# Performance work log

Measured on AMD Instinct MI355X. Metric: run time of the kernel, lower is better.

## Reference

```python
import jax, jax.numpy as jnp
import numpy as np

N_NODES = 50000
N_EDGES = 640000
HIDDEN = 128
NUM_CONVS = 3
VOCAB = 100  # nn.Embedding(100, hidden_dim)


def setup_inputs() -> dict:
    key = jax.random.key(0)
    ks = jax.random.split(key, 8)
    z = jax.random.randint(ks[0], (N_NODES,), 0, VOCAB)
    edge_index = jax.random.randint(ks[1], (2, N_EDGES), 0, N_NODES)
    edge_attr = jax.random.normal(ks[2], (N_EDGES, HIDDEN), jnp.float32)
    emb = jax.random.normal(ks[3], (VOCAB, HIDDEN), jnp.float32) * 0.02
    s = 1.0 / np.sqrt(HIDDEN)
    # Stacked per-conv MLP params: Linear(H,H) -> relu -> Linear(H,H)
    W1 = jax.random.uniform(ks[4], (NUM_CONVS, HIDDEN, HIDDEN), jnp.float32, -s, s)
    b1 = jnp.zeros((NUM_CONVS, HIDDEN), jnp.float32)
    W2 = jax.random.uniform(ks[5], (NUM_CONVS, HIDDEN, HIDDEN), jnp.float32, -s, s)
    b2 = jnp.zeros((NUM_CONVS, HIDDEN), jnp.float32)
    return dict(z=z, edge_index=edge_index, edge_attr=edge_attr,
                emb=emb, W1=W1, b1=b1, W2=W2, b2=b2)


def reference(z, edge_index, edge_attr, emb, W1, b1, W2, b2):
    x = emb[z]  # [N, H] node embeddings
    src, dst = edge_index[0], edge_index[1]
    n = x.shape[0]
    num_convs = W1.shape[0]
    for i in range(num_convs):
        # GINEConv: message = relu(x_j + edge_attr), aggr='add' at dst
        msg = jax.nn.relu(x[src] + edge_attr)                      # [E, H]
        agg = jax.ops.segment_sum(msg, dst, num_segments=n)        # [N, H]
        out = agg + x  # (1 + eps) * x_r with eps = 0
        # MultiLayerPerceptron(H, [H, H], activation='relu'): relu between layers only
        h = jax.nn.relu(out @ W1[i] + b1[i]) @ W2[i] + b2[i]
        if i < num_convs - 1:
            h = jax.nn.relu(h)  # inter-conv activation
        x = h + x  # short_cut residual
    return x  # concat_hidden=False -> last hidden
```

## Files before the change

### kernel.cpp

```cpp
#include <hip/hip_runtime.h>

#define HID 128
#define NNODE 50000
#define NEDGE 640000

static __global__ void embed_kernel(const int* __restrict__ z,
                                    const float* __restrict__ emb,
                                    float* __restrict__ x) {
  int i = blockIdx.x * 256 + threadIdx.x;
  const int total = NNODE * (HID / 4);
  if (i >= total) return;
  int node = i >> 5;
  int c = i & 31;
  ((float4*)x)[i] = ((const float4*)emb)[(size_t)z[node] * 32 + c];
}

static __global__ void hist_kernel(const int* __restrict__ dst, int* __restrict__ deg) {
  int i = blockIdx.x * 256 + threadIdx.x;
  if (i < NEDGE) atomicAdd(&deg[dst[i]], 1);
}

static __global__ void scan_kernel(const int* __restrict__ deg,
                                   int* __restrict__ row_ptr,
                                   int* __restrict__ cursor) {
  __shared__ int sums[1024];
  int t = threadIdx.x;
  const int per = (NNODE + 1023) / 1024;
  int base = t * per;
  int s = 0;
  for (int i = 0; i < per; ++i) {
    int idx = base + i;
    if (idx < NNODE) s += deg[idx];
  }
  sums[t] = s;
  __syncthreads();
  for (int off = 1; off < 1024; off <<= 1) {
    int v = (t >= off) ? sums[t - off] : 0;
    __syncthreads();
    if (t >= off) sums[t] += v;
    __syncthreads();
  }
  int run = (t == 0) ? 0 : sums[t - 1];
  for (int i = 0; i < per; ++i) {
    int idx = base + i;
    if (idx < NNODE) {
      row_ptr[idx] = run;
      cursor[idx] = run;
      run += deg[idx];
    }
  }
  if (t == 1023) row_ptr[NNODE] = run;
}

static __global__ void fill_kernel(const int* __restrict__ src, const int* __restrict__ dst,
                                   int* __restrict__ cursor, int2* __restrict__ elist) {
  int i = blockIdx.x * 256 + threadIdx.x;
  if (i < NEDGE) {
    int d = dst[i];
    int p = atomicAdd(&cursor[d], 1);
    elist[p] = make_int2(i, src[i]);
  }
}

static __global__ __launch_bounds__(256) void gather_kernel(
    const float* __restrict__ x, const float* __restrict__ ea,
    const int* __restrict__ row_ptr, const int2* __restrict__ elist,
    float* __restrict__ out) {
  int wave = threadIdx.x >> 6;
  int lane = threadIdx.x & 63;
  int node = blockIdx.x * 4 + wave;
  if (node >= NNODE) return;
  const float2* x2 = (const float2*)x;
  const float2* e2 = (const float2*)ea;
  float2 a0 = x2[(size_t)node * 64 + lane];
  float2 a1 = make_float2(0.f, 0.f);
  float2 a2 = make_float2(0.f, 0.f);
  float2 a3 = make_float2(0.f, 0.f);
  int j  = row_ptr[node];
  int je = row_ptr[node + 1];
  for (; j + 4 <= je; j += 4) {
    int2 e0 = elist[j], e1 = elist[j + 1], e2i = elist[j + 2], e3 = elist[j + 3];
    float2 xv0 = x2[(size_t)e0.y * 64 + lane];
    float2 ev0 = e2[(size_t)e0.x * 64 + lane];
    float2 xv1 = x2[(size_t)e1.y * 64 + lane];
    float2 ev1 = e2[(size_t)e1.x * 64 + lane];
    float2 xv2 = x2[(size_t)e2i.y * 64 + lane];
    float2 ev2 = e2[(size_t)e2i.x * 64 + lane];
    float2 xv3 = x2[(size_t)e3.y * 64 + lane];
    float2 ev3 = e2[(size_t)e3.x * 64 + lane];
    a0.x += fmaxf(xv0.x + ev0.x, 0.f); a0.y += fmaxf(xv0.y + ev0.y, 0.f);
    a1.x += fmaxf(xv1.x + ev1.x, 0.f); a1.y += fmaxf(xv1.y + ev1.y, 0.f);
    a2.x += fmaxf(xv2.x + ev2.x, 0.f); a2.y += fmaxf(xv2.y + ev2.y, 0.f);
    a3.x += fmaxf(xv3.x + ev3.x, 0.f); a3.y += fmaxf(xv3.y + ev3.y, 0.f);
  }
  for (; j < je; ++j) {
    int2 es = elist[j];
    float2 xv = x2[(size_t)es.y * 64 + lane];
    float2 ev = e2[(size_t)es.x * 64 + lane];
    a0.x += fmaxf(xv.x + ev.x, 0.f);
    a0.y += fmaxf(xv.y + ev.y, 0.f);
  }
  a0.x += a1.x + a2.x + a3.x;
  a0.y += a1.y + a2.y + a3.y;
  ((float2*)out)[(size_t)node * 64 + lane] = a0;
}

static __global__ __launch_bounds__(256) void mlp_kernel(
    const float* __restrict__ in, const float* __restrict__ xres,
    const float* __restrict__ W1, const float* __restrict__ b1,
    const float* __restrict__ W2, const float* __restrict__ b2,
    float* __restrict__ xout, int relu_out) {
  __shared__ float As[64 * 132];
  __shared__ float Wb[32 * 128];
  const int tid = threadIdx.x;
  const int row0 = blockIdx.x * 64;

  for (int i = tid; i < 64 * 32; i += 256) {
    int r = i >> 5, c = i & 31;
    float4 v = make_float4(0.f, 0.f, 0.f, 0.f);
    int row = row0 + r;
    if (row < NNODE) v = ((const float4*)in)[(size_t)row * 32 + c];
    *(float4*)&As[r * 132 + c * 4] = v;
  }

  const int rg = tid >> 4, cg = tid & 15;
  const int rb = rg * 4, cb = cg * 8;

  float acc[4][8];
#pragma unroll
  for (int r = 0; r < 4; ++r)
#pragma unroll
    for (int c = 0; c < 8; ++c) acc[r][c] = 0.f;

  for (int ch = 0; ch < 4; ++ch) {
    __syncthreads();
    for (int i = tid; i < 32 * 32; i += 256)
      ((float4*)Wb)[i] = ((const float4*)(W1 + ch * 32 * 128))[i];
    __syncthreads();
    const int k0 = ch * 32;
    for (int k = 0; k < 32; k += 4) {
      float4 a0 = *(const float4*)&As[(rb + 0) * 132 + k0 + k];
      float4 a1 = *(const float4*)&As[(rb + 1) * 132 + k0 + k];
      float4 a2 = *(const float4*)&As[(rb + 2) * 132 + k0 + k];
      float4 a3 = *(const float4*)&As[(rb + 3) * 132 + k0 + k];
#pragma unroll
      for (int kk = 0; kk < 4; ++kk) {
        float4 w0 = *(const float4*)&Wb[(k + kk) * 128 + cb];
        float4 w1 = *(const float4*)&Wb[(k + kk) * 128 + cb + 4];
        float av[4] = {((const float*)&a0)[kk], ((const float*)&a1)[kk],
                       ((const float*)&a2)[kk], ((const float*)&a3)[kk]};
#pragma unroll
        for (int r = 0; r < 4; ++r) {
          acc[r][0] += av[r] * w0.x; acc[r][1] += av[r] * w0.y;
          acc[r][2] += av[r] * w0.z; acc[r][3] += av[r] * w0.w;
          acc[r][4] += av[r] * w1.x; acc[r][5] += av[r] * w1.y;
          acc[r][6] += av[r] * w1.z; acc[r][7] += av[r] * w1.w;
        }
      }
    }
  }
  __syncthreads();

  {
    float4 bb0 = ((const float4*)b1)[cb >> 2];
    float4 bb1 = ((const float4*)b1)[(cb >> 2) + 1];
    float bv[8] = {bb0.x, bb0.y, bb0.z, bb0.w, bb1.x, bb1.y, bb1.z, bb1.w};
#pragma unroll
    for (int r = 0; r < 4; ++r) {
      float t0[8];
#pragma unroll
      for (int c = 0; c < 8; ++c) t0[c] = fmaxf(acc[r][c] + bv[c], 0.f);
      *(float4*)&As[(rb + r) * 132 + cb]     = make_float4(t0[0], t0[1], t0[2], t0[3]);
      *(float4*)&As[(rb + r) * 132 + cb + 4] = make_float4(t0[4], t0[5], t0[6], t0[7]);
    }
  }

#pragma unroll
  for (int r = 0; r < 4; ++r)
#pragma unroll
    for (int c = 0; c < 8; ++c) acc[r][c] = 0.f;

  for (int ch = 0; ch < 4; ++ch) {
    __syncthreads();
    for (int i = tid; i < 32 * 32; i += 256)
      ((float4*)Wb)[i] = ((const float4*)(W2 + ch * 32 * 128))[i];
    __syncthreads();
    const int k0 = ch * 32;
    for (int k = 0; k < 32; k += 4) {
      float4 a0 = *(const float4*)&As[(rb + 0) * 132 + k0 + k];
      float4 a1 = *(const float4*)&As[(rb + 1) * 132 + k0 + k];
      float4 a2 = *(const float4*)&As[(rb + 2) * 132 + k0 + k];
      float4 a3 = *(const float4*)&As[(rb + 3) * 132 + k0 + k];
#pragma unroll
      for (int kk = 0; kk < 4; ++kk) {
        float4 w0 = *(const float4*)&Wb[(k + kk) * 128 + cb];
        float4 w1 = *(const float4*)&Wb[(k + kk) * 128 + cb + 4];
        float av[4] = {((const float*)&a0)[kk], ((const float*)&a1)[kk],
                       ((const float*)&a2)[kk], ((const float*)&a3)[kk]};
#pragma unroll
        for (int r = 0; r < 4; ++r) {
          acc[r][0] += av[r] * w0.x; acc[r][1] += av[r] * w0.y;
          acc[r][2] += av[r] * w0.z; acc[r][3] += av[r] * w0.w;
          acc[r][4] += av[r] * w1.x; acc[r][5] += av[r] * w1.y;
          acc[r][6] += av[r] * w1.z; acc[r][7] += av[r] * w1.w;
        }
      }
    }
  }

  {
    float4 bb0 = ((const float4*)b2)[cb >> 2];
    float4 bb1 = ((const float4*)b2)[(cb >> 2) + 1];
    float bv[8] = {bb0.x, bb0.y, bb0.z, bb0.w, bb1.x, bb1.y, bb1.z, bb1.w};
#pragma unroll
    for (int r = 0; r < 4; ++r) {
      int row = row0 + rb + r;
      if (row < NNODE) {
        float4 xv0 = ((const float4*)xres)[(size_t)row * 32 + (cb >> 2)];
        float4 xv1 = ((const float4*)xres)[(size_t)row * 32 + (cb >> 2) + 1];
        float o[8];
#pragma unroll
        for (int c = 0; c < 8; ++c) {
          float v = acc[r][c] + bv[c];
          if (relu_out) v = fmaxf(v, 0.f);
          o[c] = v;
        }
        o[0] += xv0.x; o[1] += xv0.y; o[2] += xv0.z; o[3] += xv0.w;
        o[4] += xv1.x; o[5] += xv1.y; o[6] += xv1.z; o[7] += xv1.w;
        ((float4*)xout)[(size_t)row * 32 + (cb >> 2)]     = make_float4(o[0], o[1], o[2], o[3]);
        ((float4*)xout)[(size_t)row * 32 + (cb >> 2) + 1] = make_float4(o[4], o[5], o[6], o[7]);
      }
    }
  }
}

extern "C" void kernel_launch(void* const* d_in, const int* in_sizes, int n_in,
                              void* d_out, int out_size, void* d_ws, size_t ws_size,
                              hipStream_t stream) {
  const int*   z   = (const int*)d_in[0];
  const int*   ei  = (const int*)d_in[1];
  const float* ea  = (const float*)d_in[2];
  const float* emb = (const float*)d_in[3];
  const float* W1  = (const float*)d_in[4];
  const float* b1  = (const float*)d_in[5];
  const float* W2  = (const float*)d_in[6];
  const float* b2  = (const float*)d_in[7];
  float* outp = (float*)d_out;

  char* ws = (char*)d_ws;
  float* xbuf   = (float*)(ws + 0);
  float* obuf   = (float*)(ws + 25600000);
  int*   deg    = (int*)  (ws + 51200000);
  int*   cursor = (int*)  (ws + 51400000);
  int*   rowptr = (int*)  (ws + 51600000);
  int2*  elist  = (int2*) (ws + 51800016);

  const int* srcv = ei;
  const int* dstv = ei + NEDGE;

  hipMemsetAsync(deg, 0, NNODE * sizeof(int), stream);
  embed_kernel<<<(NNODE * 32 + 255) / 256, 256, 0, stream>>>(z, emb, xbuf);
  hist_kernel<<<(NEDGE + 255) / 256, 256, 0, stream>>>(dstv, deg);
  scan_kernel<<<1, 1024, 0, stream>>>(deg, rowptr, cursor);
  fill_kernel<<<(NEDGE + 255) / 256, 256, 0, stream>>>(srcv, dstv, cursor, elist);

  for (int i = 0; i < 3; ++i) {
    gather_kernel<<<(NNODE + 3) / 4, 256, 0, stream>>>(xbuf, ea, rowptr, elist, obuf);
    float* xo = (i == 2) ? outp : xbuf;
    mlp_kernel<<<(NNODE + 63) / 64, 256, 0, stream>>>(
        obuf, xbuf,
        W1 + (size_t)i * HID * HID, b1 + (size_t)i * HID,
        W2 + (size_t)i * HID * HID, b2 + (size_t)i * HID,
        xo, (i < 2) ? 1 : 0);
  }
}
```

Before: 1.076 ms.

## Run node MLP on bf16 MFMA with split-precision weights and activations

Result: faster. 967.5 us (-10.1%).

```diff
diff --git a/kernel.cpp b/kernel.cpp
--- a/kernel.cpp
+++ b/kernel.cpp
@@ -3,6 +3,9 @@
 #define HID 128
 #define NNODE 50000
 #define NEDGE 640000
+
+typedef __attribute__((ext_vector_type(8))) short bf16x8;
+typedef __attribute__((ext_vector_type(4))) float f32x4;
 
 static __global__ void embed_kernel(const int* __restrict__ z,
                                     const float* __restrict__ emb,
@@ -62,6 +65,25 @@
   }
 }
 
+static __global__ void wsplit_kernel(const float* __restrict__ W1, const float* __restrict__ W2,
+                                     unsigned short* __restrict__ whi,
+                                     unsigned short* __restrict__ wlo) {
+  int idx = blockIdx.x * 256 + threadIdx.x;
+  if (idx >= 6 * 16384) return;
+  int cg = idx >> 14;
+  int rem = idx & 16383;
+  int k = rem >> 7, n = rem & 127;
+  int c = cg >> 1, g = cg & 1;
+  float v = (g ? W2 : W1)[c * 16384 + k * 128 + n];
+  unsigned u = __float_as_uint(v);
+  unsigned hb = u >> 16;
+  float hf = __uint_as_float(hb << 16);
+  unsigned lb = __float_as_uint(v - hf) >> 16;
+  int o = cg * 17408 + n * 136 + k;
+  whi[o] = (unsigned short)hb;
+  wlo[o] = (unsigned short)lb;
+}
+
 static __global__ __launch_bounds__(256) void gather_kernel(
     const float* __restrict__ x, const float* __restrict__ ea,
     const int* __restrict__ row_ptr, const int2* __restrict__ elist,
@@ -71,7 +93,7 @@
   int node = blockIdx.x * 4 + wave;
   if (node >= NNODE) return;
   const float2* x2 = (const float2*)x;
-  const float2* e2 = (const float2*)ea;
+  const double* ed = (const double*)ea;
   float2 a0 = x2[(size_t)node * 64 + lane];
   float2 a1 = make_float2(0.f, 0.f);
   float2 a2 = make_float2(0.f, 0.f);
@@ -81,13 +103,15 @@
   for (; j + 4 <= je; j += 4) {
     int2 e0 = elist[j], e1 = elist[j + 1], e2i = elist[j + 2], e3 = elist[j + 3];
     float2 xv0 = x2[(size_t)e0.y * 64 + lane];
-    float2 ev0 = e2[(size_t)e0.x * 64 + lane];
+    double d0 = __builtin_nontemporal_load(&ed[(size_t)e0.x * 64 + lane]);
     float2 xv1 = x2[(size_t)e1.y * 64 + lane];
-    float2 ev1 = e2[(size_t)e1.x * 64 + lane];
+    double d1 = __builtin_nontemporal_load(&ed[(size_t)e1.x * 64 + lane]);
     float2 xv2 = x2[(size_t)e2i.y * 64 + lane];
-    float2 ev2 = e2[(size_t)e2i.x * 64 + lane];
+    double d2 = __builtin_nontemporal_load(&ed[(size_t)e2i.x * 64 + lane]);
     float2 xv3 = x2[(size_t)e3.y * 64 + lane];
-    float2 ev3 = e2[(size_t)e3.x * 64 + lane];
+    double d3 = __builtin_nontemporal_load(&ed[(size_t)e3.x * 64 + lane]);
+    float2 ev0 = *(float2*)&d0, ev1 = *(float2*)&d1;
+    float2 ev2 = *(float2*)&d2, ev3 = *(float2*)&d3;
     a0.x += fmaxf(xv0.x + ev0.x, 0.f); a0.y += fmaxf(xv0.y + ev0.y, 0.f);
     a1.x += fmaxf(xv1.x + ev1.x, 0.f); a1.y += fmaxf(xv1.y + ev1.y, 0.f);
     a2.x += fmaxf(xv2.x + ev2.x, 0.f); a2.y += fmaxf(xv2.y + ev2.y, 0.f);
@@ -96,7 +120,8 @@
   for (; j < je; ++j) {
     int2 es = elist[j];
     float2 xv = x2[(size_t)es.y * 64 + lane];
-    float2 ev = e2[(size_t)es.x * 64 + lane];
+    double d0 = __builtin_nontemporal_load(&ed[(size_t)es.x * 64 + lane]);
+    float2 ev = *(float2*)&d0;
     a0.x += fmaxf(xv.x + ev.x, 0.f);
     a0.y += fmaxf(xv.y + ev.y, 0.f);
   }
@@ -105,130 +130,123 @@
   ((float2*)out)[(size_t)node * 64 + lane] = a0;
 }
 
-static __global__ __launch_bounds__(256) void mlp_kernel(
+static __global__ __launch_bounds__(256) void mlp_mfma(
     const float* __restrict__ in, const float* __restrict__ xres,
-    const float* __restrict__ W1, const float* __restrict__ b1,
-    const float* __restrict__ W2, const float* __restrict__ b2,
+    const unsigned short* __restrict__ wt1hi, const unsigned short* __restrict__ wt1lo,
+    const unsigned short* __restrict__ wt2hi, const unsigned short* __restrict__ wt2lo,
+    const float* __restrict__ b1, const float* __restrict__ b2,
     float* __restrict__ xout, int relu_out) {
-  __shared__ float As[64 * 132];
-  __shared__ float Wb[32 * 128];
+  __shared__ unsigned short WbHi[128 * 72];
+  __shared__ unsigned short WbLo[128 * 72];
+  __shared__ float Ts[64 * 132];
   const int tid = threadIdx.x;
+  const int w = tid >> 6, l = tid & 63;
+  const int lm = l & 15, quad = l >> 4;
   const int row0 = blockIdx.x * 64;
 
-  for (int i = tid; i < 64 * 32; i += 256) {
-    int r = i >> 5, c = i & 31;
-    float4 v = make_float4(0.f, 0.f, 0.f, 0.f);
-    int row = row0 + r;
-    if (row < NNODE) v = ((const float4*)in)[(size_t)row * 32 + c];
-    *(float4*)&As[r * 132 + c * 4] = v;
-  }
-
-  const int rg = tid >> 4, cg = tid & 15;
-  const int rb = rg * 4, cb = cg * 8;
-
-  float acc[4][8];
-#pragma unroll
-  for (int r = 0; r < 4; ++r)
-#pragma unroll
-    for (int c = 0; c < 8; ++c) acc[r][c] = 0.f;
-
-  for (int ch = 0; ch < 4; ++ch) {
-    __syncthreads();
-    for (int i = tid; i < 32 * 32; i += 256)
-      ((float4*)Wb)[i] = ((const float4*)(W1 + ch * 32 * 128))[i];
-    __syncthreads();
-    const int k0 = ch * 32;
-    for (int k = 0; k < 32; k += 4) {
-      float4 a0 = *(const float4*)&As[(rb + 0) * 132 + k0 + k];
-      float4 a1 = *(const float4*)&As[(rb + 1) * 132 + k0 + k];
-      float4 a2 = *(const float4*)&As[(rb + 2) * 132 + k0 + k];
-      float4 a3 = *(const float4*)&As[(rb + 3) * 132 + k0 + k];
-#pragma unroll
-      for (int kk = 0; kk < 4; ++kk) {
-        float4 w0 = *(const float4*)&Wb[(k + kk) * 128 + cb];
-        float4 w1 = *(const float4*)&Wb[(k + kk) * 128 + cb + 4];
-        float av[4] = {((const float*)&a0)[kk], ((const float*)&a1)[kk],
-                       ((const float*)&a2)[kk], ((const float*)&a3)[kk]};
-#pragma unroll
-        for (int r = 0; r < 4; ++r) {
-          acc[r][0] += av[r] * w0.x; acc[r][1] += av[r] * w0.y;
-          acc[r][2] += av[r] * w0.z; acc[r][3] += av[r] * w0.w;
-          acc[r][4] += av[r] * w1.x; acc[r][5] += av[r] * w1.y;
-          acc[r][6] += av[r] * w1.z; acc[r][7] += av[r] * w1.w;
-        }
+  float b1v[8], b2v[8];
+#pragma unroll
+  for (int t = 0; t < 8; ++t) { b1v[t] = b1[t * 16 + lm]; b2v[t] = b2[t * 16 + lm]; }
+
+  f32x4 acc[8];
+#pragma unroll
+  for (int t = 0; t < 8; ++t) acc[t] = (f32x4){0.f, 0.f, 0.f, 0.f};
+
+  int arow = row0 + w * 16 + lm;
+  if (arow >= NNODE) arow = NNODE - 1;
+
+  for (int kc = 0; kc < 128; kc += 64) {
+    __syncthreads();
+    for (int idx = tid; idx < 128 * 8; idx += 256) {
+      int n = idx >> 3, seg = idx & 7;
+      *(uint4*)&WbHi[n * 72 + seg * 8] = *(const uint4*)&wt1hi[n * 136 + kc + seg * 8];
+      *(uint4*)&WbLo[n * 72 + seg * 8] = *(const uint4*)&wt1lo[n * 136 + kc + seg * 8];
+    }
+    __syncthreads();
+#pragma unroll
+    for (int ks = 0; ks < 64; ks += 32) {
+      const float* ap = in + (size_t)arow * 128 + kc + ks + quad * 8;
+      float4 av0 = *(const float4*)ap;
+      float4 av1 = *(const float4*)(ap + 4);
+      float av[8] = {av0.x, av0.y, av0.z, av0.w, av1.x, av1.y, av1.z, av1.w};
+      bf16x8 ah, al;
+#pragma unroll
+      for (int jj = 0; jj < 8; ++jj) {
+        unsigned u = __float_as_uint(av[jj]);
+        unsigned hb = u >> 16;
+        float hf = __uint_as_float(hb << 16);
+        unsigned lb = __float_as_uint(av[jj] - hf) >> 16;
+        ah[jj] = (short)hb; al[jj] = (short)lb;
+      }
+#pragma unroll
+      for (int t = 0; t < 8; ++t) {
+        int off = (t * 16 + lm) * 72 + ks + quad * 8;
+        bf16x8 bh = *(const bf16x8*)&WbHi[off];
+        bf16x8 bl = *(const bf16x8*)&WbLo[off];
+        acc[t] = __builtin_amdgcn_mfma_f32_16x16x32_bf16(ah, bh, acc[t], 0, 0, 0);
+        acc[t] = __builtin_amdgcn_mfma_f32_16x16x32_bf16(ah, bl, acc[t], 0, 0, 0);
+        acc[t] = __builtin_amdgcn_mfma_f32_16x16x32_bf16(al, bh, acc[t], 0, 0, 0);
       }
     }
   }
   __syncthreads();
 
-  {
-    float4 bb0 = ((const float4*)b1)[cb >> 2];
-    float4 bb1 = ((const float4*)b1)[(cb >> 2) + 1];
-    float bv[8] = {bb0.x, bb0.y, bb0.z, bb0.w, bb1.x, bb1.y, bb1.z, bb1.w};
+#pragma unroll
+  for (int t = 0; t < 8; ++t)
+#pragma unroll
+    for (int r = 0; r < 4; ++r)
+      Ts[(w * 16 + quad * 4 + r) * 132 + t * 16 + lm] = fmaxf(acc[t][r] + b1v[t], 0.f);
+
+#pragma unroll
+  for (int t = 0; t < 8; ++t) acc[t] = (f32x4){0.f, 0.f, 0.f, 0.f};
+  __syncthreads();
+
+  for (int kc = 0; kc < 128; kc += 64) {
+    __syncthreads();
+    for (int idx = tid; idx < 128 * 8; idx += 256) {
+      int n = idx >> 3, seg = idx & 7;
+      *(uint4*)&WbHi[n * 72 + seg * 8] = *(const uint4*)&wt2hi[n * 136 + kc + seg * 8];
+      *(uint4*)&WbLo[n * 72 + seg * 8] = *(const uint4*)&wt2lo[n * 136 + kc + seg * 8];
+    }
+    __syncthreads();
+#pragma unroll
+    for (int ks = 0; ks < 64; ks += 32) {
+      const float* tp = &Ts[(w * 16 + lm) * 132 + kc + ks + quad * 8];
+      float4 av0 = *(const float4*)tp;
+      float4 av1 = *(const float4*)(tp + 4);
+      float av[8] = {av0.x, av0.y, av0.z, av0.w, av1.x, av1.y, av1.z, av1.w};
+      bf16x8 ah, al;
+#pragma unroll
+      for (int jj = 0; jj < 8; ++jj) {
+        unsigned u = __float_as_uint(av[jj]);
+        unsigned hb = u >> 16;
+        float hf = __uint_as_float(hb << 16);
+        unsigned lb = __float_as_uint(av[jj] - hf) >> 16;
+        ah[jj] = (short)hb; al[jj] = (short)lb;
+      }
+#pragma unroll
+      for (int t = 0; t < 8; ++t) {
+        int off = (t * 16 + lm) * 72 + ks + quad * 8;
+        bf16x8 bh = *(const bf16x8*)&WbHi[off];
+        bf16x8 bl = *(const bf16x8*)&WbLo[off];
+        acc[t] = __builtin_amdgcn_mfma_f32_16x16x32_bf16(ah, bh, acc[t], 0, 0, 0);
+        acc[t] = __builtin_amdgcn_mfma_f32_16x16x32_bf16(ah, bl, acc[t], 0, 0, 0);
+        acc[t] = __builtin_amdgcn_mfma_f32_16x16x32_bf16(al, bh, acc[t], 0, 0, 0);
+      }
+    }
+  }
+
+#pragma unroll
+  for (int t = 0; t < 8; ++t) {
 #pragma unroll
     for (int r = 0; r < 4; ++r) {
-      float t0[8];
-#pragma unroll
-      for (int c = 0; c < 8; ++c) t0[c] = fmaxf(acc[r][c] + bv[c], 0.f);
-      *(float4*)&As[(rb + r) * 132 + cb]     = make_float4(t0[0], t0[1], t0[2], t0[3]);
-      *(float4*)&As[(rb + r) * 132 + cb + 4] = make_float4(t0[4], t0[5], t0[6], t0[7]);
-    }
-  }
-
-#pragma unroll
-  for (int r = 0; r < 4; ++r)
-#pragma unroll
-    for (int c = 0; c < 8; ++c) acc[r][c] = 0.f;
-
-  for (int ch = 0; ch < 4; ++ch) {
-    __syncthreads();
-    for (int i = tid; i < 32 * 32; i += 256)
-      ((float4*)Wb)[i] = ((const float4*)(W2 + ch * 32 * 128))[i];
-    __syncthreads();
-    const int k0 = ch * 32;
-    for (int k = 0; k < 32; k += 4) {
-      float4 a0 = *(const float4*)&As[(rb + 0) * 132 + k0 + k];
-      float4 a1 = *(const float4*)&As[(rb + 1) * 132 + k0 + k];
-      float4 a2 = *(const float4*)&As[(rb + 2) * 132 + k0 + k];
-      float4 a3 = *(const float4*)&As[(rb + 3) * 132 + k0 + k];
-#pragma unroll
-      for (int kk = 0; kk < 4; ++kk) {
-        float4 w0 = *(const float4*)&Wb[(k + kk) * 128 + cb];
-        float4 w1 = *(const float4*)&Wb[(k + kk) * 128 + cb + 4];
-        float av[4] = {((const float*)&a0)[kk], ((const float*)&a1)[kk],
-                       ((const float*)&a2)[kk], ((const float*)&a3)[kk]};
-#pragma unroll
-        for (int r = 0; r < 4; ++r) {
-          acc[r][0] += av[r] * w0.x; acc[r][1] += av[r] * w0.y;
-          acc[r][2] += av[r] * w0.z; acc[r][3] += av[r] * w0.w;
-          acc[r][4] += av[r] * w1.x; acc[r][5] += av[r] * w1.y;
-          acc[r][6] += av[r] * w1.z; acc[r][7] += av[r] * w1.w;
-        }
-      }
-    }
-  }
-
-  {
-    float4 bb0 = ((const float4*)b2)[cb >> 2];
-    float4 bb1 = ((const float4*)b2)[(cb >> 2) + 1];
-    float bv[8] = {bb0.x, bb0.y, bb0.z, bb0.w, bb1.x, bb1.y, bb1.z, bb1.w};
-#pragma unroll
-    for (int r = 0; r < 4; ++r) {
-      int row = row0 + rb + r;
+      int row = row0 + w * 16 + quad * 4 + r;
       if (row < NNODE) {
-        float4 xv0 = ((const float4*)xres)[(size_t)row * 32 + (cb >> 2)];
-        float4 xv1 = ((const float4*)xres)[(size_t)row * 32 + (cb >> 2) + 1];
-        float o[8];
-#pragma unroll
-        for (int c = 0; c < 8; ++c) {
-          float v = acc[r][c] + bv[c];
-          if (relu_out) v = fmaxf(v, 0.f);
-          o[c] = v;
-        }
-        o[0] += xv0.x; o[1] += xv0.y; o[2] += xv0.z; o[3] += xv0.w;
-        o[4] += xv1.x; o[5] += xv1.y; o[6] += xv1.z; o[7] += xv1.w;
-        ((float4*)xout)[(size_t)row * 32 + (cb >> 2)]     = make_float4(o[0], o[1], o[2], o[3]);
-        ((float4*)xout)[(size_t)row * 32 + (cb >> 2) + 1] = make_float4(o[4], o[5], o[6], o[7]);
+        int col = t * 16 + lm;
+        float v = acc[t][r] + b2v[t];
+        if (relu_out) v = fmaxf(v, 0.f);
+        v += xres[(size_t)row * 128 + col];
+        xout[(size_t)row * 128 + col] = v;
       }
     }
   }
@@ -254,6 +272,8 @@
   int*   cursor = (int*)  (ws + 51400000);
   int*   rowptr = (int*)  (ws + 51600000);
   int2*  elist  = (int2*) (ws + 51800016);
+  unsigned short* whi = (unsigned short*)(ws + 57000000);
+  unsigned short* wlo = (unsigned short*)(ws + 57250000);
 
   const int* srcv = ei;
   const int* dstv = ei + NEDGE;
@@ -263,14 +283,16 @@
   hist_kernel<<<(NEDGE + 255) / 256, 256, 0, stream>>>(dstv, deg);
   scan_kernel<<<1, 1024, 0, stream>>>(deg, rowptr, cursor);
   fill_kernel<<<(NEDGE + 255) / 256, 256, 0, stream>>>(srcv, dstv, cursor, elist);
+  wsplit_kernel<<<(6 * 16384 + 255) / 256, 256, 0, stream>>>(W1, W2, whi, wlo);
 
   for (int i = 0; i < 3; ++i) {
     gather_kernel<<<(NNODE + 3) / 4, 256, 0, stream>>>(xbuf, ea, rowptr, elist, obuf);
     float* xo = (i == 2) ? outp : xbuf;
-    mlp_kernel<<<(NNODE + 63) / 64, 256, 0, stream>>>(
+    mlp_mfma<<<(NNODE + 63) / 64, 256, 0, stream>>>(
         obuf, xbuf,
-        W1 + (size_t)i * HID * HID, b1 + (size_t)i * HID,
-        W2 + (size_t)i * HID * HID, b2 + (size_t)i * HID,
+        whi + (size_t)(i * 2 + 0) * 17408, wlo + (size_t)(i * 2 + 0) * 17408,
+        whi + (size_t)(i * 2 + 1) * 17408, wlo + (size_t)(i * 2 + 1) * 17408,
+        b1 + (size_t)i * HID, b2 + (size_t)i * HID,
         xo, (i < 2) ? 1 : 0);
   }
 }
```
